# Optimization experiments

Measured on AMD Instinct MI355X. Metric: run time of the kernel, lower is better.

## Reference

```python
import jax, jax.numpy as jnp
import numpy as np

B, S, E, H = 4, 2048, 1024, 16
D = E // H  # head_dim = 64


def setup_inputs() -> dict:
    key = jax.random.key(0)
    ks = jax.random.split(key, 7)
    scale = 1.0 / np.sqrt(E)
    inp = {
        "query": jax.random.normal(ks[0], (B, S, E), jnp.float32),
        "key": jax.random.normal(ks[1], (B, S, E), jnp.float32),
        "value": jax.random.normal(ks[2], (B, S, E), jnp.float32),
        # nn.Linear weights: [out_features, in_features]
        "Wq": jax.random.normal(ks[3], (E, E), jnp.float32) * scale,
        "Wk": jax.random.normal(ks[4], (E, E), jnp.float32) * scale,
        "Wv": jax.random.normal(ks[5], (E, E), jnp.float32) * scale,
        "Wo": jax.random.normal(ks[6], (E, E), jnp.float32) * scale,
        # broadcastable causal mask; masked_fill where mask == 0
        "mask": jnp.tril(jnp.ones((S, S), jnp.bool_))[None, None, :, :],
    }
    return inp


def reference(query, key, value, Wq, Wk, Wv, Wo, mask):
    # projections (Linear, no bias): x @ W.T
    Q = (query @ Wq.T).reshape(B, S, H, D)
    K = (key @ Wk.T).reshape(B, S, H, D)
    V = (value @ Wv.T).reshape(B, S, H, D)
    # full score matrix [B,H,S,S]
    scores = jnp.einsum("bqhd,bkhd->bhqk", Q, K) / jnp.sqrt(jnp.float32(D))
    scores = jnp.where(mask, scores, jnp.float32(-1e20))
    attn = jax.nn.softmax(scores, axis=-1)
    out = jnp.einsum("bhqk,bkhd->bqhd", attn, V).reshape(B, S, E)
    return out @ Wo.T
```

## Files before the change

kernel.cpp:

```cpp
#include <hip/hip_runtime.h>
#include <stdint.h>


#define LOG2E 1.44269504088896340736f

typedef __bf16 bf16;
typedef __attribute__((ext_vector_type(8))) __bf16 bf16x8;
typedef __attribute__((ext_vector_type(4))) __bf16 bf16x4;
typedef __attribute__((ext_vector_type(4))) float f32x4;

static constexpr int Sq = 2048, Eq = 1024;
static constexpr int Mq = 4 * Sq;

__device__ __forceinline__ f32x4 mfma16(bf16x8 a, bf16x8 b, f32x4 c) {
  return __builtin_amdgcn_mfma_f32_16x16x32_bf16(a, b, c, 0, 0, 0);
}

__device__ __forceinline__ float fexp2(float x) {
  return __builtin_amdgcn_exp2f(x);
}

__device__ __forceinline__ void gload16(const bf16* g, bf16* l) {
  __builtin_amdgcn_global_load_lds(
      (const __attribute__((address_space(1))) void*)g,
      (__attribute__((address_space(3))) void*)l, 16, 0, 0);
}

__device__ __forceinline__ bf16x8 vcat(bf16x4 lo, bf16x4 hi) {
  return __builtin_shufflevector(lo, hi, 0, 1, 2, 3, 4, 5, 6, 7);
}

__device__ __forceinline__ bf16x8 scale8(bf16x8 v, float s) {
  bf16x8 o;
#pragma unroll
  for (int i = 0; i < 8; ++i) o[i] = (bf16)((float)v[i] * s);
  return o;
}

__device__ __forceinline__ void store4(bf16* p, f32x4 a, float s) {
  bf16x4 v;
#pragma unroll
  for (int rg = 0; rg < 4; ++rg) v[rg] = (bf16)(a[rg] * s);
  *(bf16x4*)p = v;
}

__device__ __forceinline__ bf16x8 cvt8(const float4& a, const float4& b) {
  bf16x8 v;
  v[0] = (bf16)a.x; v[1] = (bf16)a.y; v[2] = (bf16)a.z; v[3] = (bf16)a.w;
  v[4] = (bf16)b.x; v[5] = (bf16)b.y; v[6] = (bf16)b.z; v[7] = (bf16)b.w;
  return v;
}

__global__ void cast_w4(const float* __restrict__ a, const float* __restrict__ b,
                        const float* __restrict__ c, const float* __restrict__ d,
                        bf16* __restrict__ oa, bf16* __restrict__ ob,
                        bf16* __restrict__ oc, bf16* __restrict__ od) {
  int i = blockIdx.x * blockDim.x + threadIdx.x;
  int sel = i >> 17, off = i & ((1 << 17) - 1);
  const float* src = sel == 0 ? a : sel == 1 ? b : sel == 2 ? c : d;
  bf16* dst = sel == 0 ? oa : sel == 1 ? ob : sel == 2 ? oc : od;
  const float4* p = (const float4*)src;
  ((bf16x8*)dst)[off] = cvt8(p[off * 2], p[off * 2 + 1]);
}

template <int MODE, int AFP32>
__global__ __launch_bounds__(256) void gemm_bt(const void* __restrict__ Ain,
                                               const bf16* __restrict__ W,
                                               void* __restrict__ Cout) {
  __shared__ __align__(16) bf16 Alds[128 * 64];
  __shared__ __align__(16) bf16 Blds[128 * 64];

  int bid = blockIdx.x;
  int nwg = gridDim.x;
  int wg = (bid & 7) * (nwg >> 3) + (bid >> 3);
  int tm = wg >> 3, tn = wg & 7;
  int tid = threadIdx.x;
  int l = tid & 63, wv = tid >> 6;
  int wm = wv >> 1, wn = wv & 1;
  int l15 = l & 15, lg = l >> 4;

  f32x4 acc[4][4] = {};
  const size_t arow = (size_t)tm * 128, brow = (size_t)tn * 128;
  const bf16* Ab = (const bf16*)Ain;
  const float* Af = (const float*)Ain;

  for (int k0 = 0; k0 < 1024; k0 += 64) {
#pragma unroll
    for (int j = 0; j < 4; ++j) {
      int loc = tid * 16 + j * 4096;
      int r = loc >> 7;
      int c = (loc & 127) >> 1;
      gload16(W + (brow + r) * 1024 + k0 + c, (bf16*)((char*)Blds + loc));
      if (!AFP32)
        gload16(Ab + (arow + r) * 1024 + k0 + c, (bf16*)((char*)Alds + loc));
    }
    if (AFP32) {
#pragma unroll
      for (int j = 0; j < 4; ++j) {
        int row = (tid >> 3) + j * 32;
        int colf = (tid & 7) * 8;
        const float4* ap =
            (const float4*)(Af + (arow + row) * 1024 + k0 + colf);
        float4 a0 = ap[0], a1 = ap[1];
        *(bf16x8*)(Alds + row * 64 + colf) = cvt8(a0, a1);
      }
    }
    __syncthreads();
#pragma unroll
    for (int kk = 0; kk < 2; ++kk) {
      bf16x8 af[4], bfr[4];
#pragma unroll
      for (int t = 0; t < 4; ++t) {
        int ma = wm * 64 + t * 16 + l15;
        af[t] = *(const bf16x8*)((const char*)Alds + ma * 128 + 16 * lg + 64 * kk);
        int nb = wn * 64 + t * 16 + l15;
        bfr[t] = *(const bf16x8*)((const char*)Blds + nb * 128 + 16 * lg + 64 * kk);
      }
#pragma unroll
      for (int mt = 0; mt < 4; ++mt)
#pragma unroll
        for (int nt = 0; nt < 4; ++nt)
          acc[mt][nt] = mfma16(af[mt], bfr[nt], acc[mt][nt]);
    }
    __syncthreads();
  }

  int mbase = tm * 128 + wm * 64;
  int nbase = tn * 128 + wn * 64;
  if (MODE == 0 || MODE == 2) {
#pragma unroll
    for (int mt = 0; mt < 4; ++mt) {
#pragma unroll
      for (int nt = 0; nt < 4; ++nt) {
        int m0 = mbase + mt * 16 + (lg << 2);
        int n = nbase + nt * 16 + l15;
#pragma unroll
        for (int rg = 0; rg < 4; ++rg) {
          if (MODE == 0)
            ((bf16*)Cout)[(size_t)(m0 + rg) * 1024 + n] = (bf16)acc[mt][nt][rg];
          else
            ((float*)Cout)[(size_t)(m0 + rg) * 1024 + n] = acc[mt][nt][rg];
        }
      }
    }
  } else {
#pragma unroll
    for (int mt = 0; mt < 4; ++mt) {
#pragma unroll
      for (int nt = 0; nt < 4; ++nt) {
        int m0 = mbase + mt * 16 + (lg << 2);
        int n = nbase + nt * 16 + l15;
        bf16x4 vv;
#pragma unroll
        for (int rg = 0; rg < 4; ++rg) vv[rg] = (bf16)acc[mt][nt][rg];
        int bb = m0 >> 11, s0 = m0 & 2047;
        size_t off = ((size_t)((bb * 16 + (n >> 6)) * 64 + (n & 63))) * 2048 + s0;
        *(bf16x4*)((bf16*)Cout + off) = vv;
      }
    }
  }
}

__global__ __launch_bounds__(256) void attn_kernel(
    const bf16* __restrict__ Qp, const bf16* __restrict__ Kp,
    const bf16* __restrict__ Vt, bf16* __restrict__ AO) {
  __shared__ __align__(16) bf16 sm[2][2][4096];

  int bid = blockIdx.x;
  int qb = 15 - (bid >> 6);
  int bh = ((bid & 7) << 3) | ((bid >> 3) & 7);
  int b = bh >> 4, h = bh & 15;
  int tid = threadIdx.x;
  int w = tid >> 6, l = tid & 63;
  int l15 = l & 15, lg = l >> 4;

  int qw0 = qb * 128 + w * 32;
  int cdiag = qw0 >> 6;
  int nc = (qb + 1) * 2;
  int qg0 = qw0 + l15, qg1 = qw0 + 16 + l15;

  const float sc = 0.125f * LOG2E;
  bf16 one1 = (bf16)1.0f;
  bf16x8 ones = {one1, one1, one1, one1, one1, one1, one1, one1};

  const bf16* qp_ = Qp + (size_t)(b * 2048 + qw0 + l15) * 1024 + h * 64 + 8 * lg;
  bf16x8 q00 = scale8(*(const bf16x8*)qp_, sc);
  bf16x8 q01 = scale8(*(const bf16x8*)(qp_ + 32), sc);
  bf16x8 q10 = scale8(*(const bf16x8*)(qp_ + 16384), sc);
  bf16x8 q11 = scale8(*(const bf16x8*)(qp_ + 16384 + 32), sc);

  const bf16* Kbase = Kp + (size_t)(b * 2048) * 1024 + h * 64;
  const bf16* Vbase = Vt + (size_t)(bh * 64) * 2048;

  f32x4 r0 = {0.f, 0.f, 0.f, 0.f}, r1 = r0;
  f32x4 o0[4] = {}, o1[4] = {};

#define STAGE(c_, bufp)                                                     \
  do {                                                                      \
    int _c = (c_);                                                          \
    _Pragma("unroll") for (int j = 0; j < 2; ++j) {                         \
      int loc = tid * 16 + j * 4096;                                        \
      int row = loc >> 7, u = (loc >> 4) & 7;                               \
      int sel = (u ^ (row & 7)) << 3;                                       \
      gload16(Kbase + (size_t)(_c * 64 + row) * 1024 + sel,                 \
              (bf16*)((char*)sm[bufp][0] + loc));                           \
      gload16(Vbase + (size_t)row * 2048 + _c * 64 + sel,                   \
              (bf16*)((char*)sm[bufp][1] + loc));                           \
    }                                                                       \
  } while (0)

  STAGE(0, 0);
  __syncthreads();
  int cur = 0;
  for (int c = 0; c < nc; ++c) {
    if (c + 1 < nc) STAGE(c + 1, cur ^ 1);
    if (c <= cdiag) {
      const char* lK = (const char*)sm[cur][0];
      const char* lV = (const char*)sm[cur][1];
      const f32x4 cinit = {-6.f, -6.f, -6.f, -6.f};
      f32x4 s0[4], s1[4];
#pragma unroll
      for (int kt = 0; kt < 4; ++kt) {
        int row = kt * 16 + l15, sw = (row & 7) << 4;
        const char* kb = lK + row * 128;
        bf16x8 kf0 = *(const bf16x8*)(kb + ((lg * 16) ^ sw));
        bf16x8 kf1 = *(const bf16x8*)(kb + ((64 + lg * 16) ^ sw));
        s0[kt] = mfma16(kf1, q01, mfma16(kf0, q00, cinit));
        s1[kt] = mfma16(kf1, q11, mfma16(kf0, q10, cinit));
      }
      if (c == cdiag) {
#pragma unroll
        for (int kt = 0; kt < 4; ++kt)
#pragma unroll
          for (int rg = 0; rg < 4; ++rg) {
            int kg = c * 64 + kt * 16 + 4 * lg + rg;
            if (kg > qg0) s0[kt][rg] = -1e30f;
            if (kg > qg1) s1[kt][rg] = -1e30f;
          }
      }
      bf16x8 plo0, phi0, plo1, phi1;
#pragma unroll
      for (int rg = 0; rg < 4; ++rg) {
        plo0[rg] = (bf16)fexp2(s0[0][rg]); plo0[rg + 4] = (bf16)fexp2(s0[1][rg]);
        phi0[rg] = (bf16)fexp2(s0[2][rg]); phi0[rg + 4] = (bf16)fexp2(s0[3][rg]);
        plo1[rg] = (bf16)fexp2(s1[0][rg]); plo1[rg + 4] = (bf16)fexp2(s1[1][rg]);
        phi1[rg] = (bf16)fexp2(s1[2][rg]); phi1[rg + 4] = (bf16)fexp2(s1[3][rg]);
      }
      r0 = mfma16(ones, phi0, mfma16(ones, plo0, r0));
      r1 = mfma16(ones, phi1, mfma16(ones, plo1, r1));
#pragma unroll
      for (int dt = 0; dt < 4; ++dt) {
        int row = dt * 16 + l15, sw = (row & 7) << 4;
        const char* vb = lV + row * 128;
        bf16x8 vf0 = vcat(*(const bf16x4*)(vb + ((lg * 8) ^ sw)),
                          *(const bf16x4*)(vb + ((32 + lg * 8) ^ sw)));
        bf16x8 vf1 = vcat(*(const bf16x4*)(vb + ((64 + lg * 8) ^ sw)),
                          *(const bf16x4*)(vb + ((96 + lg * 8) ^ sw)));
        o0[dt] = mfma16(vf1, phi0, mfma16(vf0, plo0, o0[dt]));
        o1[dt] = mfma16(vf1, phi1, mfma16(vf0, plo1, o1[dt]));
      }
    }
    __syncthreads();
    cur ^= 1;
  }
#undef STAGE

  float inv0 = 1.0f / r0[0], inv1 = 1.0f / r1[0];
  bf16* ob = AO + (size_t)(b * 2048 + qw0 + l15) * 1024 + h * 64 + 4 * lg;
#pragma unroll
  for (int dt = 0; dt < 4; ++dt) {
    store4(ob + dt * 16, o0[dt], inv0);
    store4(ob + 16384 + dt * 16, o1[dt], inv1);
  }
}

extern "C" void kernel_launch(void* const* d_in, const int* in_sizes, int n_in,
                              void* d_out, int out_size, void* d_ws, size_t ws_size,
                              hipStream_t stream) {
  (void)in_sizes; (void)n_in; (void)out_size; (void)ws_size;
  const float* dq = (const float*)d_in[0];
  const float* dk = (const float*)d_in[1];
  const float* dv = (const float*)d_in[2];
  const float* wq = (const float*)d_in[3];
  const float* wk = (const float*)d_in[4];
  const float* wv = (const float*)d_in[5];
  const float* wo = (const float*)d_in[6];

  char* ws = (char*)d_ws;
  const size_t MB = 1u << 20;
  bf16* AO  = (bf16*)(ws + 0 * MB);
  bf16* wqb = (bf16*)(ws + 48 * MB);
  bf16* wkb = (bf16*)(ws + 50 * MB);
  bf16* wvb = (bf16*)(ws + 52 * MB);
  bf16* wob = (bf16*)(ws + 54 * MB);
  bf16* Qp  = (bf16*)(ws + 56 * MB);
  bf16* Kp  = (bf16*)(ws + 72 * MB);
  bf16* Vt  = (bf16*)(ws + 88 * MB);

  cast_w4<<<4 * 512, 256, 0, stream>>>(wq, wk, wv, wo, wqb, wkb, wvb, wob);

  gemm_bt<0, 1><<<512, 256, 0, stream>>>(dq, wqb, (void*)Qp);
  gemm_bt<0, 1><<<512, 256, 0, stream>>>(dk, wkb, (void*)Kp);
  gemm_bt<1, 1><<<512, 256, 0, stream>>>(dv, wvb, (void*)Vt);
  attn_kernel<<<1024, 256, 0, stream>>>(Qp, Kp, Vt, AO);
  gemm_bt<2, 0><<<512, 256, 0, stream>>>(AO, wob, d_out);
}
```

Before: 195.9 us.

## Fuse QKV projections, pair causal query blocks per workgroup, permute V layout

Merges the three Q/K/V projection GEMMs into one launch with 1536 workgroups, so fewer launches and better fill of the GPU. The attention kernel now gives each workgroup a short query block and its mirrored long block (j and 15-j), which balances causal work across 512 workgroups instead of 1024 uneven ones. The K/V tile for the second pass is prefetched while the first pass ends. V is written in a permuted sequence order so each lane reads one 16-byte LDS load instead of two 8-byte loads. The trade-off is a longer, serial loop per workgroup and more complex index logic.

Result: faster. 187.3 us (-4.4%).

```diff
diff --git a/kernel.cpp b/kernel.cpp
--- a/kernel.cpp
+++ b/kernel.cpp
@@ -10,7 +10,6 @@
 typedef __attribute__((ext_vector_type(4))) float f32x4;
 
 static constexpr int Sq = 2048, Eq = 1024;
-static constexpr int Mq = 4 * Sq;
 
 __device__ __forceinline__ f32x4 mfma16(bf16x8 a, bf16x8 b, f32x4 c) {
   return __builtin_amdgcn_mfma_f32_16x16x32_bf16(a, b, c, 0, 0, 0);
@@ -24,10 +23,6 @@
   __builtin_amdgcn_global_load_lds(
       (const __attribute__((address_space(1))) void*)g,
       (__attribute__((address_space(3))) void*)l, 16, 0, 0);
-}
-
-__device__ __forceinline__ bf16x8 vcat(bf16x4 lo, bf16x4 hi) {
-  return __builtin_shufflevector(lo, hi, 0, 1, 2, 3, 4, 5, 6, 7);
 }
 
 __device__ __forceinline__ bf16x8 scale8(bf16x8 v, float s) {
@@ -63,6 +58,99 @@
   ((bf16x8*)dst)[off] = cvt8(p[off * 2], p[off * 2 + 1]);
 }
 
+__global__ __launch_bounds__(256) void gemm_qkv(
+    const float* __restrict__ Aq, const float* __restrict__ Ak,
+    const float* __restrict__ Av, const bf16* __restrict__ Wq,
+    const bf16* __restrict__ Wk, const bf16* __restrict__ Wv,
+    bf16* __restrict__ Qp, bf16* __restrict__ Kp, bf16* __restrict__ Vt) {
+  __shared__ __align__(16) bf16 Alds[128 * 64];
+  __shared__ __align__(16) bf16 Blds[128 * 64];
+
+  int bid = blockIdx.x;
+  int which = bid >> 9;
+  int sub = bid & 511;
+  const float* Af = which == 0 ? Aq : which == 1 ? Ak : Av;
+  const bf16* W = which == 0 ? Wq : which == 1 ? Wk : Wv;
+
+  int wg = (sub & 7) * 64 + (sub >> 3);
+  int tm = wg >> 3, tn = wg & 7;
+  int tid = threadIdx.x;
+  int l = tid & 63, wv = tid >> 6;
+  int wm = wv >> 1, wn = wv & 1;
+  int l15 = l & 15, lg = l >> 4;
+
+  f32x4 acc[4][4] = {};
+  const size_t arow = (size_t)tm * 128, brow = (size_t)tn * 128;
+
+  for (int k0 = 0; k0 < 1024; k0 += 64) {
+#pragma unroll
+    for (int j = 0; j < 4; ++j) {
+      int loc = tid * 16 + j * 4096;
+      int r = loc >> 7;
+      int c = (loc & 127) >> 1;
+      gload16(W + (brow + r) * 1024 + k0 + c, (bf16*)((char*)Blds + loc));
+    }
+#pragma unroll
+    for (int j = 0; j < 4; ++j) {
+      int row = (tid >> 3) + j * 32;
+      int colf = (tid & 7) * 8;
+      const float4* ap = (const float4*)(Af + (arow + row) * 1024 + k0 + colf);
+      float4 a0 = ap[0], a1 = ap[1];
+      *(bf16x8*)(Alds + row * 64 + colf) = cvt8(a0, a1);
+    }
+    __syncthreads();
+#pragma unroll
+    for (int kk = 0; kk < 2; ++kk) {
+      bf16x8 af[4], bfr[4];
+#pragma unroll
+      for (int t = 0; t < 4; ++t) {
+        int ma = wm * 64 + t * 16 + l15;
+        af[t] = *(const bf16x8*)((const char*)Alds + ma * 128 + 16 * lg + 64 * kk);
+        int nb = wn * 64 + t * 16 + l15;
+        bfr[t] = *(const bf16x8*)((const char*)Blds + nb * 128 + 16 * lg + 64 * kk);
+      }
+#pragma unroll
+      for (int mt = 0; mt < 4; ++mt)
+#pragma unroll
+        for (int nt = 0; nt < 4; ++nt)
+          acc[mt][nt] = mfma16(af[mt], bfr[nt], acc[mt][nt]);
+    }
+    __syncthreads();
+  }
+
+  int mbase = tm * 128 + wm * 64;
+  int nbase = tn * 128 + wn * 64;
+  if (which < 2) {
+    bf16* C = which == 0 ? Qp : Kp;
+#pragma unroll
+    for (int mt = 0; mt < 4; ++mt)
+#pragma unroll
+      for (int nt = 0; nt < 4; ++nt) {
+        int m0 = mbase + mt * 16 + (lg << 2);
+        int n = nbase + nt * 16 + l15;
+#pragma unroll
+        for (int rg = 0; rg < 4; ++rg)
+          C[(size_t)(m0 + rg) * 1024 + n] = (bf16)acc[mt][nt][rg];
+      }
+  } else {
+#pragma unroll
+    for (int mt = 0; mt < 4; ++mt)
+#pragma unroll
+      for (int nt = 0; nt < 4; ++nt) {
+        int m0 = mbase + mt * 16 + (lg << 2);
+        int n = nbase + nt * 16 + l15;
+        bf16x4 vv;
+#pragma unroll
+        for (int rg = 0; rg < 4; ++rg) vv[rg] = (bf16)acc[mt][nt][rg];
+        int bb = m0 >> 11, s0 = m0 & 2047;
+        int sp = (s0 & ~31) | (((s0 >> 4) & 1) << 2) | (((s0 >> 2) & 3) << 3);
+        size_t off =
+            ((size_t)((bb * 16 + (n >> 6)) * 64 + (n & 63))) * 2048 + sp;
+        *(bf16x4*)(Vt + off) = vv;
+      }
+  }
+}
+
 template <int MODE, int AFP32>
 __global__ __launch_bounds__(256) void gemm_bt(const void* __restrict__ Ain,
                                                const bf16* __restrict__ W,
@@ -99,8 +187,7 @@
       for (int j = 0; j < 4; ++j) {
         int row = (tid >> 3) + j * 32;
         int colf = (tid & 7) * 8;
-        const float4* ap =
-            (const float4*)(Af + (arow + row) * 1024 + k0 + colf);
+        const float4* ap = (const float4*)(Af + (arow + row) * 1024 + k0 + colf);
         float4 a0 = ap[0], a1 = ap[1];
         *(bf16x8*)(Alds + row * 64 + colf) = cvt8(a0, a1);
       }
@@ -127,38 +214,20 @@
 
   int mbase = tm * 128 + wm * 64;
   int nbase = tn * 128 + wn * 64;
-  if (MODE == 0 || MODE == 2) {
-#pragma unroll
-    for (int mt = 0; mt < 4; ++mt) {
-#pragma unroll
-      for (int nt = 0; nt < 4; ++nt) {
-        int m0 = mbase + mt * 16 + (lg << 2);
-        int n = nbase + nt * 16 + l15;
-#pragma unroll
-        for (int rg = 0; rg < 4; ++rg) {
-          if (MODE == 0)
-            ((bf16*)Cout)[(size_t)(m0 + rg) * 1024 + n] = (bf16)acc[mt][nt][rg];
-          else
-            ((float*)Cout)[(size_t)(m0 + rg) * 1024 + n] = acc[mt][nt][rg];
-        }
-      }
-    }
-  } else {
-#pragma unroll
-    for (int mt = 0; mt < 4; ++mt) {
-#pragma unroll
-      for (int nt = 0; nt < 4; ++nt) {
-        int m0 = mbase + mt * 16 + (lg << 2);
-        int n = nbase + nt * 16 + l15;
-        bf16x4 vv;
-#pragma unroll
-        for (int rg = 0; rg < 4; ++rg) vv[rg] = (bf16)acc[mt][nt][rg];
-        int bb = m0 >> 11, s0 = m0 & 2047;
-        size_t off = ((size_t)((bb * 16 + (n >> 6)) * 64 + (n & 63))) * 2048 + s0;
-        *(bf16x4*)((bf16*)Cout + off) = vv;
-      }
-    }
-  }
+#pragma unroll
+  for (int mt = 0; mt < 4; ++mt)
+#pragma unroll
+    for (int nt = 0; nt < 4; ++nt) {
+      int m0 = mbase + mt * 16 + (lg << 2);
+      int n = nbase + nt * 16 + l15;
+#pragma unroll
+      for (int rg = 0; rg < 4; ++rg) {
+        if (MODE == 0)
+          ((bf16*)Cout)[(size_t)(m0 + rg) * 1024 + n] = (bf16)acc[mt][nt][rg];
+        else
+          ((float*)Cout)[(size_t)(m0 + rg) * 1024 + n] = acc[mt][nt][rg];
+      }
+    }
 }
 
 __global__ __launch_bounds__(256) void attn_kernel(
@@ -167,39 +236,38 @@
   __shared__ __align__(16) bf16 sm[2][2][4096];
 
   int bid = blockIdx.x;
-  int qb = 15 - (bid >> 6);
   int bh = ((bid & 7) << 3) | ((bid >> 3) & 7);
+  int j = bid >> 6;
   int b = bh >> 4, h = bh & 15;
   int tid = threadIdx.x;
   int w = tid >> 6, l = tid & 63;
   int l15 = l & 15, lg = l >> 4;
 
-  int qw0 = qb * 128 + w * 32;
-  int cdiag = qw0 >> 6;
-  int nc = (qb + 1) * 2;
-  int qg0 = qw0 + l15, qg1 = qw0 + 16 + l15;
-
+  int ncA = 2 * j + 2, ncB = 32 - 2 * j;
   const float sc = 0.125f * LOG2E;
   bf16 one1 = (bf16)1.0f;
   bf16x8 ones = {one1, one1, one1, one1, one1, one1, one1, one1};
 
+  const bf16* Kbase = Kp + (size_t)(b * 2048) * 1024 + h * 64;
+  const bf16* Vbase = Vt + (size_t)(bh * 64) * 2048;
+
+  int qw0 = j * 128 + w * 32;
+  int cdiag = 2 * j + (w >> 1);
+  int qg0 = qw0 + l15, qg1 = qw0 + 16 + l15;
   const bf16* qp_ = Qp + (size_t)(b * 2048 + qw0 + l15) * 1024 + h * 64 + 8 * lg;
   bf16x8 q00 = scale8(*(const bf16x8*)qp_, sc);
   bf16x8 q01 = scale8(*(const bf16x8*)(qp_ + 32), sc);
   bf16x8 q10 = scale8(*(const bf16x8*)(qp_ + 16384), sc);
   bf16x8 q11 = scale8(*(const bf16x8*)(qp_ + 16384 + 32), sc);
 
-  const bf16* Kbase = Kp + (size_t)(b * 2048) * 1024 + h * 64;
-  const bf16* Vbase = Vt + (size_t)(bh * 64) * 2048;
-
   f32x4 r0 = {0.f, 0.f, 0.f, 0.f}, r1 = r0;
   f32x4 o0[4] = {}, o1[4] = {};
 
 #define STAGE(c_, bufp)                                                     \
   do {                                                                      \
     int _c = (c_);                                                          \
-    _Pragma("unroll") for (int j = 0; j < 2; ++j) {                         \
-      int loc = tid * 16 + j * 4096;                                        \
+    _Pragma("unroll") for (int jj = 0; jj < 2; ++jj) {                      \
+      int loc = tid * 16 + jj * 4096;                                       \
       int row = loc >> 7, u = (loc >> 4) & 7;                               \
       int sel = (u ^ (row & 7)) << 3;                                       \
       gload16(Kbase + (size_t)(_c * 64 + row) * 1024 + sel,                 \
@@ -209,69 +277,93 @@
     }                                                                       \
   } while (0)
 
+#define CHUNKC(c_)                                                          \
+  do {                                                                      \
+    const int _c = (c_);                                                    \
+    const char* lK = (const char*)sm[cur][0];                               \
+    const char* lV = (const char*)sm[cur][1];                               \
+    const f32x4 cinit = {-6.f, -6.f, -6.f, -6.f};                           \
+    f32x4 s0[4], s1[4];                                                     \
+    _Pragma("unroll") for (int kt = 0; kt < 4; ++kt) {                      \
+      int row = kt * 16 + l15, sw = (row & 7) << 4;                         \
+      const char* kb = lK + row * 128;                                      \
+      bf16x8 kf0 = *(const bf16x8*)(kb + ((lg * 16) ^ sw));                 \
+      bf16x8 kf1 = *(const bf16x8*)(kb + ((64 + lg * 16) ^ sw));            \
+      s0[kt] = mfma16(kf1, q01, mfma16(kf0, q00, cinit));                   \
+      s1[kt] = mfma16(kf1, q11, mfma16(kf0, q10, cinit));                   \
+    }                                                                       \
+    if (_c == cdiag) {                                                      \
+      _Pragma("unroll") for (int kt = 0; kt < 4; ++kt)                      \
+          _Pragma("unroll") for (int rg = 0; rg < 4; ++rg) {                \
+        int kg = _c * 64 + kt * 16 + 4 * lg + rg;                           \
+        if (kg > qg0) s0[kt][rg] = -1e30f;                                  \
+        if (kg > qg1) s1[kt][rg] = -1e30f;                                  \
+      }                                                                     \
+    }                                                                       \
+    bf16x8 plo0, phi0, plo1, phi1;                                          \
+    _Pragma("unroll") for (int rg = 0; rg < 4; ++rg) {                      \
+      plo0[rg] = (bf16)fexp2(s0[0][rg]); plo0[rg + 4] = (bf16)fexp2(s0[1][rg]); \
+      phi0[rg] = (bf16)fexp2(s0[2][rg]); phi0[rg + 4] = (bf16)fexp2(s0[3][rg]); \
+      plo1[rg] = (bf16)fexp2(s1[0][rg]); plo1[rg + 4] = (bf16)fexp2(s1[1][rg]); \
+      phi1[rg] = (bf16)fexp2(s1[2][rg]); phi1[rg + 4] = (bf16)fexp2(s1[3][rg]); \
+    }                                                                       \
+    r0 = mfma16(ones, phi0, mfma16(ones, plo0, r0));                        \
+    r1 = mfma16(ones, phi1, mfma16(ones, plo1, r1));                        \
+    _Pragma("unroll") for (int dt = 0; dt < 4; ++dt) {                      \
+      int row = dt * 16 + l15, sw = (row & 7) << 4;                         \
+      const char* vb = lV + row * 128;                                      \
+      bf16x8 vf0 = *(const bf16x8*)(vb + ((lg * 16) ^ sw));                 \
+      bf16x8 vf1 = *(const bf16x8*)(vb + ((64 + lg * 16) ^ sw));            \
+      o0[dt] = mfma16(vf1, phi0, mfma16(vf0, plo0, o0[dt]));                \
+      o1[dt] = mfma16(vf1, phi1, mfma16(vf0, plo1, o1[dt]));                \
+    }                                                                       \
+  } while (0)
+
+#define STOREOUT()                                                          \
+  do {                                                                      \
+    float inv0 = 1.0f / r0[0], inv1 = 1.0f / r1[0];                         \
+    bf16* ob = AO + (size_t)(b * 2048 + qw0 + l15) * 1024 + h * 64 + 4 * lg; \
+    _Pragma("unroll") for (int dt = 0; dt < 4; ++dt) {                      \
+      store4(ob + dt * 16, o0[dt], inv0);                                   \
+      store4(ob + 16384 + dt * 16, o1[dt], inv1);                           \
+    }                                                                       \
+  } while (0)
+
   STAGE(0, 0);
   __syncthreads();
   int cur = 0;
-  for (int c = 0; c < nc; ++c) {
-    if (c + 1 < nc) STAGE(c + 1, cur ^ 1);
-    if (c <= cdiag) {
-      const char* lK = (const char*)sm[cur][0];
-      const char* lV = (const char*)sm[cur][1];
-      const f32x4 cinit = {-6.f, -6.f, -6.f, -6.f};
-      f32x4 s0[4], s1[4];
-#pragma unroll
-      for (int kt = 0; kt < 4; ++kt) {
-        int row = kt * 16 + l15, sw = (row & 7) << 4;
-        const char* kb = lK + row * 128;
-        bf16x8 kf0 = *(const bf16x8*)(kb + ((lg * 16) ^ sw));
-        bf16x8 kf1 = *(const bf16x8*)(kb + ((64 + lg * 16) ^ sw));
-        s0[kt] = mfma16(kf1, q01, mfma16(kf0, q00, cinit));
-        s1[kt] = mfma16(kf1, q11, mfma16(kf0, q10, cinit));
-      }
-      if (c == cdiag) {
-#pragma unroll
-        for (int kt = 0; kt < 4; ++kt)
-#pragma unroll
-          for (int rg = 0; rg < 4; ++rg) {
-            int kg = c * 64 + kt * 16 + 4 * lg + rg;
-            if (kg > qg0) s0[kt][rg] = -1e30f;
-            if (kg > qg1) s1[kt][rg] = -1e30f;
-          }
-      }
-      bf16x8 plo0, phi0, plo1, phi1;
-#pragma unroll
-      for (int rg = 0; rg < 4; ++rg) {
-        plo0[rg] = (bf16)fexp2(s0[0][rg]); plo0[rg + 4] = (bf16)fexp2(s0[1][rg]);
-        phi0[rg] = (bf16)fexp2(s0[2][rg]); phi0[rg + 4] = (bf16)fexp2(s0[3][rg]);
-        plo1[rg] = (bf16)fexp2(s1[0][rg]); plo1[rg + 4] = (bf16)fexp2(s1[1][rg]);
-        phi1[rg] = (bf16)fexp2(s1[2][rg]); phi1[rg + 4] = (bf16)fexp2(s1[3][rg]);
-      }
-      r0 = mfma16(ones, phi0, mfma16(ones, plo0, r0));
-      r1 = mfma16(ones, phi1, mfma16(ones, plo1, r1));
-#pragma unroll
-      for (int dt = 0; dt < 4; ++dt) {
-        int row = dt * 16 + l15, sw = (row & 7) << 4;
-        const char* vb = lV + row * 128;
-        bf16x8 vf0 = vcat(*(const bf16x4*)(vb + ((lg * 8) ^ sw)),
-                          *(const bf16x4*)(vb + ((32 + lg * 8) ^ sw)));
-        bf16x8 vf1 = vcat(*(const bf16x4*)(vb + ((64 + lg * 8) ^ sw)),
-                          *(const bf16x4*)(vb + ((96 + lg * 8) ^ sw)));
-        o0[dt] = mfma16(vf1, phi0, mfma16(vf0, plo0, o0[dt]));
-        o1[dt] = mfma16(vf1, phi1, mfma16(vf0, plo1, o1[dt]));
-      }
-    }
+
+  for (int c = 0; c < ncA; ++c) {
+    int g = c + 1;
+    STAGE(g < ncA ? g : g - ncA, cur ^ 1);
+    if (c <= cdiag) CHUNKC(c);
     __syncthreads();
     cur ^= 1;
   }
+  STOREOUT();
+
+  qw0 = (15 - j) * 128 + w * 32;
+  cdiag = 2 * (15 - j) + (w >> 1);
+  qg0 = qw0 + l15; qg1 = qw0 + 16 + l15;
+  qp_ = Qp + (size_t)(b * 2048 + qw0 + l15) * 1024 + h * 64 + 8 * lg;
+  q00 = scale8(*(const bf16x8*)qp_, sc);
+  q01 = scale8(*(const bf16x8*)(qp_ + 32), sc);
+  q10 = scale8(*(const bf16x8*)(qp_ + 16384), sc);
+  q11 = scale8(*(const bf16x8*)(qp_ + 16384 + 32), sc);
+  r0 = f32x4{0.f, 0.f, 0.f, 0.f}; r1 = r0;
+#pragma unroll
+  for (int dt = 0; dt < 4; ++dt) { o0[dt] = r0; o1[dt] = r0; }
+
+  for (int c = 0; c < ncB; ++c) {
+    if (c + 1 < ncB) STAGE(c + 1, cur ^ 1);
+    if (c <= cdiag) CHUNKC(c);
+    __syncthreads();
+    cur ^= 1;
+  }
+  STOREOUT();
 #undef STAGE
-
-  float inv0 = 1.0f / r0[0], inv1 = 1.0f / r1[0];
-  bf16* ob = AO + (size_t)(b * 2048 + qw0 + l15) * 1024 + h * 64 + 4 * lg;
-#pragma unroll
-  for (int dt = 0; dt < 4; ++dt) {
-    store4(ob + dt * 16, o0[dt], inv0);
-    store4(ob + 16384 + dt * 16, o1[dt], inv1);
-  }
+#undef CHUNKC
+#undef STOREOUT
 }
 
 extern "C" void kernel_launch(void* const* d_in, const int* in_sizes, int n_in,
@@ -298,10 +390,7 @@
   bf16* Vt  = (bf16*)(ws + 88 * MB);
 
   cast_w4<<<4 * 512, 256, 0, stream>>>(wq, wk, wv, wo, wqb, wkb, wvb, wob);
-
-  gemm_bt<0, 1><<<512, 256, 0, stream>>>(dq, wqb, (void*)Qp);
-  gemm_bt<0, 1><<<512, 256, 0, stream>>>(dk, wkb, (void*)Kp);
-  gemm_bt<1, 1><<<512, 256, 0, stream>>>(dv, wvb, (void*)Vt);
-  attn_kernel<<<1024, 256, 0, stream>>>(Qp, Kp, Vt, AO);
+  gemm_qkv<<<1536, 256, 0, stream>>>(dq, dk, dv, wqb, wkb, wvb, Qp, Kp, Vt);
+  attn_kernel<<<512, 256, 0, stream>>>(Qp, Kp, Vt, AO);
   gemm_bt<2, 0><<<512, 256, 0, stream>>>(AO, wob, d_out);
 }
```
